# Performance work log

Measured on AMD Instinct MI355X. Metric: run time of the kernel, lower is better.

The kernel has to match this reference:

```python
import jax, jax.numpy as jnp
import numpy as np

B, N, L, H, N_NODE, STEP = 1024, 64, 64, 128, 50000, 2


def setup_inputs() -> dict:
    key = jax.random.key(0)
    ks = jax.random.split(key, 24)
    stdv = 1.0 / np.sqrt(H)
    u = lambda k, shape: jax.random.uniform(k, shape, jnp.float32, -stdv, stdv)
    emb = u(ks[0], (N_NODE + 1, H))
    emb = emb.at[0].set(0.0)  # padding_idx=0
    return {
        "A": jax.random.uniform(ks[1], (B, N, 2 * N), jnp.float32),
        "items": jax.random.randint(ks[2], (B, N), 0, N_NODE + 1, jnp.int32),
        "mask": jnp.ones((B, L), jnp.int32),
        "alias_input": jax.random.randint(ks[3], (B, L), 0, N, jnp.int32),
        "emb": emb,
        "w_in": u(ks[4], (H, H)), "b_in": u(ks[5], (H,)),
        "w_out": u(ks[6], (H, H)), "b_out": u(ks[7], (H,)),
        "b_iah": u(ks[8], (H,)), "b_oah": u(ks[9], (H,)),
        "wi": u(ks[10], (3 * H, 2 * H)), "bi": u(ks[11], (3 * H,)),
        "wh": u(ks[12], (3 * H, H)), "bh": u(ks[13], (3 * H,)),
        "w1": u(ks[14], (H, H)), "b1": u(ks[15], (H,)),
        "w2": u(ks[16], (H, H)), "b2": u(ks[17], (H,)),
        "wq": u(ks[18], (1, H)),
        "w3": u(ks[19], (H, 2 * H)), "b3": u(ks[20], (2 * H,))[:H],
    }


def _gru_cell(A, hidden, p):
    n = A.shape[1]
    h_in = hidden @ p["w_in"].T + p["b_in"]
    h_out = hidden @ p["w_out"].T + p["b_out"]
    input_in = jnp.einsum("bnm,bmh->bnh", A[:, :, :n], h_in) + p["b_iah"]
    input_out = jnp.einsum("bnm,bmh->bnh", A[:, :, n:], h_out) + p["b_oah"]
    input_emb = jnp.concatenate([input_in, input_out], axis=2)  # [B,N,2H]
    gi = input_emb @ p["wi"].T + p["bi"]
    gh = hidden @ p["wh"].T + p["bh"]
    i_r, i_i, i_n = jnp.split(gi, 3, axis=2)
    h_r, h_i, h_n = jnp.split(gh, 3, axis=2)
    update_gate = jax.nn.sigmoid(i_i + h_i)
    reset_gate = jax.nn.sigmoid(i_r + h_r)
    new_gate = jnp.tanh(reset_gate * h_n + i_n)
    return (1.0 - update_gate) * hidden + update_gate * new_gate


def reference(A, items, mask, alias_input, emb, w_in, b_in, w_out, b_out,
              b_iah, b_oah, wi, bi, wh, bh, w1, b1, w2, b2, wq, w3, b3):
    p = dict(w_in=w_in, b_in=b_in, w_out=w_out, b_out=b_out, b_iah=b_iah,
             b_oah=b_oah, wi=wi, bi=bi, wh=wh, bh=bh)
    hidden = emb[items]  # [B,N,H]
    for _ in range(STEP):
        hidden = _gru_cell(A, hidden, p)
    # gather session order: seq_hidden[b, l] = hidden[b, alias_input[b, l]]
    seq_hidden = jnp.take_along_axis(hidden, alias_input[:, :, None], axis=1)  # [B,L,H]
    last = jnp.sum(mask, axis=1) - 1  # [B]
    local_emb = jnp.take_along_axis(seq_hidden, last[:, None, None], axis=1)[:, 0]  # [B,H]
    q1 = (local_emb @ w1.T + b1)[:, None, :]
    q2 = seq_hidden @ w2.T + b2
    alpha = jax.nn.sigmoid(q1 + q2) @ wq.T  # [B,L,1]
    global_emb = jnp.sum(alpha * seq_hidden * mask[:, :, None].astype(seq_hidden.dtype), axis=1)
    return jnp.concatenate([local_emb, global_emb], axis=1) @ w3.T + b3
```

## Files before the change

### kernel.cpp

```cpp
#include <hip/hip_runtime.h>
#include <stdint.h>


#define BDIM 256
#define NB   1024
#define NN   64
#define HH   128
#define SH_STR 136
#define SX_STR 264

#define OFS_WIN  0
#define OFS_WOUT 16384
#define OFS_WI   32768
#define OFS_WH   131072
#define OFS_W2   180224
#define N_FRAGS  24576

typedef short v8s __attribute__((ext_vector_type(8)));
typedef float v4f __attribute__((ext_vector_type(4)));

__device__ __forceinline__ float b2f_lo(uint32_t u){
  union { uint32_t u; float f; } v; v.u = u << 16; return v.f;
}
__device__ __forceinline__ float b2f_hi(uint32_t u){
  union { uint32_t u; float f; } v; v.u = u & 0xffff0000u; return v.f;
}
__device__ __forceinline__ uint16_t f2b(float f){
  union { float f; uint32_t u; } v; v.f = f;
  uint32_t r = v.u + 0x7fffu + ((v.u >> 16) & 1u);
  return (uint16_t)(r >> 16);
}
__device__ __forceinline__ float b2f(uint16_t s){
  union { uint32_t u; float f; } v; v.u = ((uint32_t)s) << 16; return v.f;
}
__device__ __forceinline__ float sig_f(float x){ return 1.0f / (1.0f + __expf(-x)); }
__device__ __forceinline__ float tanh_f(float x){ return 1.0f - 2.0f / (__expf(2.0f*x) + 1.0f); }

__device__ __forceinline__ uint32_t pack2bf(float a, float b){
  union { float f; uint32_t u; } ua, ub; ua.f = a; ub.f = b;
  return __builtin_amdgcn_perm(ub.u + 0x8000u, ua.u + 0x8000u, 0x07060302u);
}

__device__ __forceinline__ v8s pack8(const float* __restrict__ p){
  float4 f0 = *reinterpret_cast<const float4*>(p);
  float4 f1 = *reinterpret_cast<const float4*>(p + 4);
  union { uint32_t u[4]; v8s v; } o;
  o.u[0] = pack2bf(f0.x, f0.y);
  o.u[1] = pack2bf(f0.z, f0.w);
  o.u[2] = pack2bf(f1.x, f1.y);
  o.u[3] = pack2bf(f1.z, f1.w);
  return o.v;
}

__device__ __forceinline__ v8s ldsA(const uint16_t* buf, int stride,
                                    int row_base, int k_base, int r, int q){
  return *reinterpret_cast<const v8s*>(&buf[(row_base + r) * stride + k_base + q * 8]);
}

__device__ __forceinline__ v8s ldfrag(const uint16_t* __restrict__ ws,
                                      int base, int tile, int lane){
  return *reinterpret_cast<const v8s*>(ws + base + (((size_t)tile * 64 + lane) << 3));
}

#define MFMA(a, b, c) __builtin_amdgcn_mfma_f32_16x16x32_bf16((a), (b), (c), 0, 0, 0)

__global__ __launch_bounds__(256) void pack_weights(
    const float* __restrict__ w_in, const float* __restrict__ w_out,
    const float* __restrict__ wi,   const float* __restrict__ wh,
    const float* __restrict__ w2,   uint16_t* __restrict__ ws)
{
  int gid = blockIdx.x * blockDim.x + threadIdx.x;
  if (gid >= N_FRAGS) return;
  const float* W; int C; int fi; int base;
  if (gid < 2048)       { W = w_in;  C = 128; fi = gid;         base = OFS_WIN; }
  else if (gid < 4096)  { W = w_out; C = 128; fi = gid - 2048;  base = OFS_WOUT; }
  else if (gid < 16384) { W = wi;    C = 256; fi = gid - 4096;  base = OFS_WI; }
  else if (gid < 22528) { W = wh;    C = 128; fi = gid - 16384; base = OFS_WH; }
  else                  { W = w2;    C = 128; fi = gid - 22528; base = OFS_W2; }
  int lane = fi & 63;
  int tile = fi >> 6;
  int tc   = C >> 5;
  int tr   = tile / tc, kc = tile - tr * tc;
  int r = lane & 15, q = lane >> 4;
  const float* p = W + (size_t)(tr * 16 + r) * C + kc * 32 + q * 8;
  *reinterpret_cast<v8s*>(ws + base + ((size_t)fi << 3)) = pack8(p);
}

__global__ __launch_bounds__(BDIM, 3) void srgnn_kernel(
    const float* __restrict__ A,
    const int*   __restrict__ items,
    const int*   __restrict__ mask,
    const int*   __restrict__ alias_input,
    const float* __restrict__ emb,
    const float* __restrict__ b_in,  const float* __restrict__ b_out,
    const float* __restrict__ b_iah, const float* __restrict__ b_oah,
    const float* __restrict__ bi,    const float* __restrict__ bh,
    const float* __restrict__ w1,    const float* __restrict__ b1,
    const float* __restrict__ b2,
    const float* __restrict__ wq,
    const float* __restrict__ w3,    const float* __restrict__ b3,
    const uint16_t* __restrict__ ws,
    float* __restrict__ out)
{
  __shared__ __align__(16) uint16_t sH[NN * SH_STR];
  __shared__ __align__(16) uint16_t sX[NN * SX_STR];
  __shared__ int sAliasRow[64], sMaskArr[64];

  float* sF      = reinterpret_cast<float*>(sX);
  float* sQ1v    = sF;
  float* sGlobv  = sF + 128;
  float* sAPartv = sF + 256;
  float* sAlphav = sF + 512;
  float* sP      = sF + 576;

  const int t    = threadIdx.x;
  const int b    = blockIdx.x;
  const int lane = t & 63;
  const int wv   = __builtin_amdgcn_readfirstlane(t >> 6);
  const int r    = lane & 15;
  const int q    = lane >> 4;

  {
    const int* itb = items + b * NN;
    for (int j = t; j < NN * HH; j += BDIM) {
      int n = j >> 7, k = j & 127;
      sH[n * SH_STR + k] = f2b(emb[(size_t)itb[n] * HH + k]);
    }
    if (t < 64) {
      sAliasRow[t] = alias_input[b * 64 + t];
      sMaskArr[t]  = mask[b * 64 + t];
    }
  }

  v8s a2[4][2];
  {
    const int half = wv >> 1;
    #pragma unroll
    for (int mt = 0; mt < 4; ++mt)
      #pragma unroll
      for (int kk = 0; kk < 2; ++kk)
        a2[mt][kk] = pack8(A + (size_t)(b * NN + mt * 16 + r) * (2 * NN)
                             + half * 64 + kk * 32 + q * 8);
  }
  __syncthreads();

  for (int step = 0; step < 2; ++step) {
    {
      v8s a[4][4];
      #pragma unroll
      for (int mt = 0; mt < 4; ++mt)
        #pragma unroll
        for (int kk = 0; kk < 4; ++kk)
          a[mt][kk] = ldsA(sH, SH_STR, mt * 16, kk * 32, r, q);

      const int    wbase = (wv < 2) ? OFS_WIN : OFS_WOUT;
      const float* bsel  = (wv < 2) ? b_in : b_out;
      const int    ntofs = (wv < 2) ? 0 : 8;
      #pragma unroll 2
      for (int i = 0; i < 4; ++i) {
        int nt = wv * 4 + i;
        int tr = nt - ntofs;
        int c  = nt * 16 + r;
        float bini = bsel[tr * 16 + r];
        v4f acc0 = {bini, bini, bini, bini}, acc1 = acc0, acc2 = acc0, acc3 = acc0;
        #pragma unroll
        for (int kk = 0; kk < 4; ++kk) {
          v8s bf = ldfrag(ws, wbase, tr * 4 + kk, lane);
          acc0 = MFMA(a[0][kk], bf, acc0);
          acc1 = MFMA(a[1][kk], bf, acc1);
          acc2 = MFMA(a[2][kk], bf, acc2);
          acc3 = MFMA(a[3][kk], bf, acc3);
        }
        #pragma unroll
        for (int reg = 0; reg < 4; ++reg) {
          sX[(0  + q * 4 + reg) * SX_STR + c] = f2b(acc0[reg]);
          sX[(16 + q * 4 + reg) * SX_STR + c] = f2b(acc1[reg]);
          sX[(32 + q * 4 + reg) * SX_STR + c] = f2b(acc2[reg]);
          sX[(48 + q * 4 + reg) * SX_STR + c] = f2b(acc3[reg]);
        }
      }
    }

    {
      const float* bsel2 = (wv < 2) ? b_iah : b_oah;
      const int    wofs2 = (wv < 2) ? 0 : 128;
      #pragma unroll 1
      for (int i = 0; i < 4; ++i) {
        int nt = wv * 4 + i;
        int c  = nt * 16 + r;
        v8s b0, b1f;
        #pragma unroll
        for (int j = 0; j < 8; ++j) {
          b0[j]  = (short)sX[(q * 8 + j) * SX_STR + c];
          b1f[j] = (short)sX[(32 + q * 8 + j) * SX_STR + c];
        }
        float bini = bsel2[c - wofs2];
        v4f acc0 = {bini, bini, bini, bini}, acc1 = acc0, acc2 = acc0, acc3 = acc0;
        acc0 = MFMA(a2[0][0], b0, acc0); acc0 = MFMA(a2[0][1], b1f, acc0);
        acc1 = MFMA(a2[1][0], b0, acc1); acc1 = MFMA(a2[1][1], b1f, acc1);
        acc2 = MFMA(a2[2][0], b0, acc2); acc2 = MFMA(a2[2][1], b1f, acc2);
        acc3 = MFMA(a2[3][0], b0, acc3); acc3 = MFMA(a2[3][1], b1f, acc3);
        #pragma unroll
        for (int reg = 0; reg < 4; ++reg) {
          sX[(0  + q * 4 + reg) * SX_STR + c] = f2b(acc0[reg]);
          sX[(16 + q * 4 + reg) * SX_STR + c] = f2b(acc1[reg]);
          sX[(32 + q * 4 + reg) * SX_STR + c] = f2b(acc2[reg]);
          sX[(48 + q * 4 + reg) * SX_STR + c] = f2b(acc3[reg]);
        }
      }
    }
    __syncthreads();

    {
      const int h0 = wv * 32;
      uint32_t nhpk[2][8];

      #pragma unroll 1
      for (int u = 0; u < 2; ++u) {
        int h = h0 + u * 16 + r;
        float vR  = bi[h] + bh[h];
        float vI  = bi[128 + h] + bh[128 + h];
        float vNi = bi[256 + h];
        float vNh = bh[256 + h];
        v4f aR[4], aI[4], aNi[4], aNh[4];
        #pragma unroll
        for (int mt = 0; mt < 4; ++mt) {
          aR[mt]  = (v4f){vR, vR, vR, vR};
          aI[mt]  = (v4f){vI, vI, vI, vI};
          aNi[mt] = (v4f){vNi, vNi, vNi, vNi};
          aNh[mt] = (v4f){vNh, vNh, vNh, vNh};
        }
        const int trb = wv * 2 + u;
        #pragma unroll 2
        for (int kk = 0; kk < 8; ++kk) {
          v8s af0 = ldsA(sX, SX_STR, 0,  kk * 32, r, q);
          v8s af1 = ldsA(sX, SX_STR, 16, kk * 32, r, q);
          v8s af2 = ldsA(sX, SX_STR, 32, kk * 32, r, q);
          v8s af3 = ldsA(sX, SX_STR, 48, kk * 32, r, q);
          v8s bR = ldfrag(ws, OFS_WI, (0 * 8 + trb) * 8 + kk, lane);
          v8s bI = ldfrag(ws, OFS_WI, (8 + trb) * 8 + kk, lane);
          v8s bN = ldfrag(ws, OFS_WI, (16 + trb) * 8 + kk, lane);
          aR[0]  = MFMA(af0, bR, aR[0]);  aR[1]  = MFMA(af1, bR, aR[1]);
          aR[2]  = MFMA(af2, bR, aR[2]);  aR[3]  = MFMA(af3, bR, aR[3]);
          aI[0]  = MFMA(af0, bI, aI[0]);  aI[1]  = MFMA(af1, bI, aI[1]);
          aI[2]  = MFMA(af2, bI, aI[2]);  aI[3]  = MFMA(af3, bI, aI[3]);
          aNi[0] = MFMA(af0, bN, aNi[0]); aNi[1] = MFMA(af1, bN, aNi[1]);
          aNi[2] = MFMA(af2, bN, aNi[2]); aNi[3] = MFMA(af3, bN, aNi[3]);
        }
        #pragma unroll 2
        for (int kk = 0; kk < 4; ++kk) {
          v8s af0 = ldsA(sH, SH_STR, 0,  kk * 32, r, q);
          v8s af1 = ldsA(sH, SH_STR, 16, kk * 32, r, q);
          v8s af2 = ldsA(sH, SH_STR, 32, kk * 32, r, q);
          v8s af3 = ldsA(sH, SH_STR, 48, kk * 32, r, q);
          v8s bR = ldfrag(ws, OFS_WH, (0 * 8 + trb) * 4 + kk, lane);
          v8s bI = ldfrag(ws, OFS_WH, (8 + trb) * 4 + kk, lane);
          v8s bN = ldfrag(ws, OFS_WH, (16 + trb) * 4 + kk, lane);
          aR[0]  = MFMA(af0, bR, aR[0]);  aR[1]  = MFMA(af1, bR, aR[1]);
          aR[2]  = MFMA(af2, bR, aR[2]);  aR[3]  = MFMA(af3, bR, aR[3]);
          aI[0]  = MFMA(af0, bI, aI[0]);  aI[1]  = MFMA(af1, bI, aI[1]);
          aI[2]  = MFMA(af2, bI, aI[2]);  aI[3]  = MFMA(af3, bI, aI[3]);
          aNh[0] = MFMA(af0, bN, aNh[0]); aNh[1] = MFMA(af1, bN, aNh[1]);
          aNh[2] = MFMA(af2, bN, aNh[2]); aNh[3] = MFMA(af3, bN, aNh[3]);
        }
        #pragma unroll
        for (int mt = 0; mt < 4; ++mt) {
          #pragma unroll
          for (int rp = 0; rp < 2; ++rp) {
            uint32_t pk = 0;
            #pragma unroll
            for (int e = 0; e < 2; ++e) {
              int reg = rp * 2 + e;
              int row = mt * 16 + q * 4 + reg;
              float z  = sig_f(aI[mt][reg]);
              float rr = sig_f(aR[mt][reg]);
              float gg = tanh_f(fmaf(rr, aNh[mt][reg], aNi[mt][reg]));
              float hp = b2f(sH[row * SH_STR + h]);
              pk |= (uint32_t)f2b(fmaf(z, gg - hp, hp)) << (16 * e);
            }
            nhpk[u][mt * 2 + rp] = pk;
          }
        }
      }
      __syncthreads();

      #pragma unroll
      for (int u = 0; u < 2; ++u) {
        int h = h0 + u * 16 + r;
        #pragma unroll
        for (int mt = 0; mt < 4; ++mt)
          #pragma unroll
          for (int rp = 0; rp < 2; ++rp) {
            uint32_t pk = nhpk[u][mt * 2 + rp];
            int row = mt * 16 + q * 4 + rp * 2;
            sH[row * SH_STR + h]       = (uint16_t)(pk & 0xffff);
            sH[(row + 1) * SH_STR + h] = (uint16_t)(pk >> 16);
          }
      }
    }
    __syncthreads();
  }

  int msum = 0;
  #pragma unroll
  for (int l = 0; l < 64; ++l) msum += sMaskArr[l];
  const int lastRow = sAliasRow[msum - 1];
  const int hh  = t & 127;
  const int seg = t >> 7;

  {
    const float4* w14 = reinterpret_cast<const float4*>(w1 + (size_t)hh * HH + seg * 64);
    const uint2*  lr  = reinterpret_cast<const uint2*>(&sH[lastRow * SH_STR + seg * 64]);
    float a0 = seg ? 0.f : b1[hh], a1 = 0.f, a2v = 0.f, a3 = 0.f;
    #pragma unroll 8
    for (int j = 0; j < 16; ++j) {
      float4 w = w14[j]; uint2 v = lr[j];
      a0  = fmaf(b2f_lo(v.x), w.x, a0);  a1 = fmaf(b2f_hi(v.x), w.y, a1);
      a2v = fmaf(b2f_lo(v.y), w.z, a2v); a3 = fmaf(b2f_hi(v.y), w.w, a3);
    }
    sP[seg * 128 + hh] = (a0 + a1) + (a2v + a3);
  }
  __syncthreads();
  if (t < HH) sQ1v[t] = sP[t] + sP[128 + t];
  __syncthreads();

  {
    v8s a[4][4];
    #pragma unroll
    for (int mt = 0; mt < 4; ++mt) {
      int row = sAliasRow[mt * 16 + r];
      #pragma unroll
      for (int kk = 0; kk < 4; ++kk)
        a[mt][kk] = *reinterpret_cast<const v8s*>(&sH[row * SH_STR + kk * 32 + q * 8]);
    }
    float part[16];
    #pragma unroll
    for (int i = 0; i < 16; ++i) part[i] = 0.f;
    #pragma unroll
    for (int u = 0; u < 2; ++u) {
      int h = wv * 32 + u * 16 + r;
      float binit = sQ1v[h] + b2[h];
      v4f acc[4];
      #pragma unroll
      for (int mt = 0; mt < 4; ++mt) acc[mt] = (v4f){binit, binit, binit, binit};
      #pragma unroll
      for (int kk = 0; kk < 4; ++kk) {
        v8s bf = ldfrag(ws, OFS_W2, (wv * 2 + u) * 4 + kk, lane);
        acc[0] = MFMA(a[0][kk], bf, acc[0]);
        acc[1] = MFMA(a[1][kk], bf, acc[1]);
        acc[2] = MFMA(a[2][kk], bf, acc[2]);
        acc[3] = MFMA(a[3][kk], bf, acc[3]);
      }
      float wqh = wq[h];
      #pragma unroll
      for (int mt = 0; mt < 4; ++mt)
        #pragma unroll
        for (int reg = 0; reg < 4; ++reg)
          part[mt * 4 + reg] += sig_f(acc[mt][reg]) * wqh;
    }
    #pragma unroll
    for (int m = 1; m <= 8; m <<= 1)
      #pragma unroll
      for (int i = 0; i < 16; ++i)
        part[i] += __shfl_xor(part[i], m);
    if (r == 0) {
      #pragma unroll
      for (int mt = 0; mt < 4; ++mt)
        #pragma unroll
        for (int reg = 0; reg < 4; ++reg)
          sAPartv[wv * 64 + mt * 16 + q * 4 + reg] = part[mt * 4 + reg];
    }
  }
  __syncthreads();
  if (t < 64) {
    sAlphav[t] = (sAPartv[t] + sAPartv[64 + t] + sAPartv[128 + t] + sAPartv[192 + t])
               * (float)sMaskArr[t];
  }
  __syncthreads();

  {
    float acc = 0.0f;
    #pragma unroll
    for (int l = 0; l < 32; ++l) {
      int ll = seg * 32 + l;
      acc = fmaf(sAlphav[ll], b2f(sH[sAliasRow[ll] * SH_STR + hh]), acc);
    }
    sP[seg * 128 + hh] = acc;
  }
  __syncthreads();
  if (t < HH) sGlobv[t] = sP[t] + sP[128 + t];
  __syncthreads();

  {
    const float4* w34 = reinterpret_cast<const float4*>(w3 + (size_t)hh * 256 + seg * 128);
    float a0 = seg ? 0.f : b3[hh], a1 = 0.f, a2v = 0.f, a3 = 0.f;
    if (seg == 0) {
      const uint2* lr = reinterpret_cast<const uint2*>(&sH[lastRow * SH_STR]);
      #pragma unroll 8
      for (int j = 0; j < 32; ++j) {
        float4 w = w34[j]; uint2 v = lr[j];
        a0  = fmaf(b2f_lo(v.x), w.x, a0);  a1 = fmaf(b2f_hi(v.x), w.y, a1);
        a2v = fmaf(b2f_lo(v.y), w.z, a2v); a3 = fmaf(b2f_hi(v.y), w.w, a3);
      }
    } else {
      #pragma unroll 8
      for (int j = 0; j < 32; ++j) {
        float4 w = w34[j];
        a0  = fmaf(sGlobv[4*j+0], w.x, a0);  a1 = fmaf(sGlobv[4*j+1], w.y, a1);
        a2v = fmaf(sGlobv[4*j+2], w.z, a2v); a3 = fmaf(sGlobv[4*j+3], w.w, a3);
      }
    }
    sP[seg * 128 + hh] = (a0 + a1) + (a2v + a3);
  }
  __syncthreads();
  if (t < HH) out[b * HH + t] = sP[t] + sP[128 + t];
}

extern "C" void kernel_launch(void* const* d_in, const int* in_sizes, int n_in,
                              void* d_out, int out_size, void* d_ws, size_t ws_size,
                              hipStream_t stream) {
  const float* A          = (const float*)d_in[0];
  const int*   items      = (const int*)  d_in[1];
  const int*   mask       = (const int*)  d_in[2];
  const int*   alias_in   = (const int*)  d_in[3];
  const float* emb        = (const float*)d_in[4];
  const float* w_in       = (const float*)d_in[5];
  const float* b_in       = (const float*)d_in[6];
  const float* w_out      = (const float*)d_in[7];
  const float* b_out      = (const float*)d_in[8];
  const float* b_iah      = (const float*)d_in[9];
  const float* b_oah      = (const float*)d_in[10];
  const float* wi         = (const float*)d_in[11];
  const float* bi         = (const float*)d_in[12];
  const float* wh         = (const float*)d_in[13];
  const float* bh         = (const float*)d_in[14];
  const float* w1         = (const float*)d_in[15];
  const float* b1         = (const float*)d_in[16];
  const float* w2         = (const float*)d_in[17];
  const float* b2         = (const float*)d_in[18];
  const float* wq         = (const float*)d_in[19];
  const float* w3         = (const float*)d_in[20];
  const float* b3         = (const float*)d_in[21];
  float* out = (float*)d_out;
  uint16_t* wsp = (uint16_t*)d_ws;

  hipLaunchKernelGGL(pack_weights, dim3((N_FRAGS + 255) / 256), dim3(256), 0, stream,
                     w_in, w_out, wi, wh, w2, wsp);
  hipLaunchKernelGGL(srgnn_kernel, dim3(NB), dim3(BDIM), 0, stream,
                     A, items, mask, alias_in, emb,
                     b_in, b_out, b_iah, b_oah, bi, bh,
                     w1, b1, b2, wq, w3, b3, wsp, out);
}
```

Baseline: 255.3 us.

## Double block to 512 threads, splitting GRU and tail work across eight waves

Raises the block from four to eight waves and repartitions every stage. Each wave now owns half as many output column tiles in the projection and GRU gate GEMMs, and the w1, alpha and w3 tails are split into four segments with matching shared-memory reductions. The aim is more waves per block to hide MFMA, LDS and global-load latency while each wave uses fewer registers. The cost is that each wave reloads the same A fragments from LDS, adds reduction and barrier overhead, and occupancy now depends on whether six 512-thread blocks actually fit per CU.

After: 385.5 us. +51.0%, slower.

```diff
diff --git a/kernel.cpp b/kernel.cpp
--- a/kernel.cpp
+++ b/kernel.cpp
@@ -2,7 +2,7 @@
 #include <stdint.h>
 
 
-#define BDIM 256
+#define BDIM 512
 #define NB   1024
 #define NN   64
 #define HH   128
@@ -86,7 +86,7 @@
   *reinterpret_cast<v8s*>(ws + base + ((size_t)fi << 3)) = pack8(p);
 }
 
-__global__ __launch_bounds__(BDIM, 3) void srgnn_kernel(
+__global__ __launch_bounds__(BDIM, 6) void srgnn_kernel(
     const float* __restrict__ A,
     const int*   __restrict__ items,
     const int*   __restrict__ mask,
@@ -110,8 +110,8 @@
   float* sQ1v    = sF;
   float* sGlobv  = sF + 128;
   float* sAPartv = sF + 256;
-  float* sAlphav = sF + 512;
-  float* sP      = sF + 576;
+  float* sAlphav = sF + 768;
+  float* sP      = sF + 832;
 
   const int t    = threadIdx.x;
   const int b    = blockIdx.x;
@@ -134,7 +134,7 @@
 
   v8s a2[4][2];
   {
-    const int half = wv >> 1;
+    const int half = wv >> 2;
     #pragma unroll
     for (int mt = 0; mt < 4; ++mt)
       #pragma unroll
@@ -153,12 +153,12 @@
         for (int kk = 0; kk < 4; ++kk)
           a[mt][kk] = ldsA(sH, SH_STR, mt * 16, kk * 32, r, q);
 
-      const int    wbase = (wv < 2) ? OFS_WIN : OFS_WOUT;
-      const float* bsel  = (wv < 2) ? b_in : b_out;
-      const int    ntofs = (wv < 2) ? 0 : 8;
-      #pragma unroll 2
-      for (int i = 0; i < 4; ++i) {
-        int nt = wv * 4 + i;
+      const int    wbase = (wv < 4) ? OFS_WIN : OFS_WOUT;
+      const float* bsel  = (wv < 4) ? b_in : b_out;
+      const int    ntofs = (wv < 4) ? 0 : 8;
+      #pragma unroll
+      for (int i = 0; i < 2; ++i) {
+        int nt = wv * 2 + i;
         int tr = nt - ntofs;
         int c  = nt * 16 + r;
         float bini = bsel[tr * 16 + r];
@@ -182,11 +182,11 @@
     }
 
     {
-      const float* bsel2 = (wv < 2) ? b_iah : b_oah;
-      const int    wofs2 = (wv < 2) ? 0 : 128;
+      const float* bsel2 = (wv < 4) ? b_iah : b_oah;
+      const int    wofs2 = (wv < 4) ? 0 : 128;
       #pragma unroll 1
-      for (int i = 0; i < 4; ++i) {
-        int nt = wv * 4 + i;
+      for (int i = 0; i < 2; ++i) {
+        int nt = wv * 2 + i;
         int c  = nt * 16 + r;
         v8s b0, b1f;
         #pragma unroll
@@ -212,91 +212,83 @@
     __syncthreads();
 
     {
-      const int h0 = wv * 32;
-      uint32_t nhpk[2][8];
-
-      #pragma unroll 1
-      for (int u = 0; u < 2; ++u) {
-        int h = h0 + u * 16 + r;
-        float vR  = bi[h] + bh[h];
-        float vI  = bi[128 + h] + bh[128 + h];
-        float vNi = bi[256 + h];
-        float vNh = bh[256 + h];
-        v4f aR[4], aI[4], aNi[4], aNh[4];
-        #pragma unroll
-        for (int mt = 0; mt < 4; ++mt) {
-          aR[mt]  = (v4f){vR, vR, vR, vR};
-          aI[mt]  = (v4f){vI, vI, vI, vI};
-          aNi[mt] = (v4f){vNi, vNi, vNi, vNi};
-          aNh[mt] = (v4f){vNh, vNh, vNh, vNh};
-        }
-        const int trb = wv * 2 + u;
-        #pragma unroll 2
-        for (int kk = 0; kk < 8; ++kk) {
-          v8s af0 = ldsA(sX, SX_STR, 0,  kk * 32, r, q);
-          v8s af1 = ldsA(sX, SX_STR, 16, kk * 32, r, q);
-          v8s af2 = ldsA(sX, SX_STR, 32, kk * 32, r, q);
-          v8s af3 = ldsA(sX, SX_STR, 48, kk * 32, r, q);
-          v8s bR = ldfrag(ws, OFS_WI, (0 * 8 + trb) * 8 + kk, lane);
-          v8s bI = ldfrag(ws, OFS_WI, (8 + trb) * 8 + kk, lane);
-          v8s bN = ldfrag(ws, OFS_WI, (16 + trb) * 8 + kk, lane);
-          aR[0]  = MFMA(af0, bR, aR[0]);  aR[1]  = MFMA(af1, bR, aR[1]);
-          aR[2]  = MFMA(af2, bR, aR[2]);  aR[3]  = MFMA(af3, bR, aR[3]);
-          aI[0]  = MFMA(af0, bI, aI[0]);  aI[1]  = MFMA(af1, bI, aI[1]);
-          aI[2]  = MFMA(af2, bI, aI[2]);  aI[3]  = MFMA(af3, bI, aI[3]);
-          aNi[0] = MFMA(af0, bN, aNi[0]); aNi[1] = MFMA(af1, bN, aNi[1]);
-          aNi[2] = MFMA(af2, bN, aNi[2]); aNi[3] = MFMA(af3, bN, aNi[3]);
-        }
-        #pragma unroll 2
-        for (int kk = 0; kk < 4; ++kk) {
-          v8s af0 = ldsA(sH, SH_STR, 0,  kk * 32, r, q);
-          v8s af1 = ldsA(sH, SH_STR, 16, kk * 32, r, q);
-          v8s af2 = ldsA(sH, SH_STR, 32, kk * 32, r, q);
-          v8s af3 = ldsA(sH, SH_STR, 48, kk * 32, r, q);
-          v8s bR = ldfrag(ws, OFS_WH, (0 * 8 + trb) * 4 + kk, lane);
-          v8s bI = ldfrag(ws, OFS_WH, (8 + trb) * 4 + kk, lane);
-          v8s bN = ldfrag(ws, OFS_WH, (16 + trb) * 4 + kk, lane);
-          aR[0]  = MFMA(af0, bR, aR[0]);  aR[1]  = MFMA(af1, bR, aR[1]);
-          aR[2]  = MFMA(af2, bR, aR[2]);  aR[3]  = MFMA(af3, bR, aR[3]);
-          aI[0]  = MFMA(af0, bI, aI[0]);  aI[1]  = MFMA(af1, bI, aI[1]);
-          aI[2]  = MFMA(af2, bI, aI[2]);  aI[3]  = MFMA(af3, bI, aI[3]);
-          aNh[0] = MFMA(af0, bN, aNh[0]); aNh[1] = MFMA(af1, bN, aNh[1]);
-          aNh[2] = MFMA(af2, bN, aNh[2]); aNh[3] = MFMA(af3, bN, aNh[3]);
-        }
-        #pragma unroll
-        for (int mt = 0; mt < 4; ++mt) {
+      const int trb = wv;
+      const int h   = wv * 16 + r;
+      uint32_t nhpk[8];
+
+      float vR  = bi[h] + bh[h];
+      float vI  = bi[128 + h] + bh[128 + h];
+      float vNi = bi[256 + h];
+      float vNh = bh[256 + h];
+      v4f aR[4], aI[4], aNi[4], aNh[4];
+      #pragma unroll
+      for (int mt = 0; mt < 4; ++mt) {
+        aR[mt]  = (v4f){vR, vR, vR, vR};
+        aI[mt]  = (v4f){vI, vI, vI, vI};
+        aNi[mt] = (v4f){vNi, vNi, vNi, vNi};
+        aNh[mt] = (v4f){vNh, vNh, vNh, vNh};
+      }
+      #pragma unroll 2
+      for (int kk = 0; kk < 8; ++kk) {
+        v8s af0 = ldsA(sX, SX_STR, 0,  kk * 32, r, q);
+        v8s af1 = ldsA(sX, SX_STR, 16, kk * 32, r, q);
+        v8s af2 = ldsA(sX, SX_STR, 32, kk * 32, r, q);
+        v8s af3 = ldsA(sX, SX_STR, 48, kk * 32, r, q);
+        v8s bR = ldfrag(ws, OFS_WI, (0 * 8 + trb) * 8 + kk, lane);
+        v8s bI = ldfrag(ws, OFS_WI, (8 + trb) * 8 + kk, lane);
+        v8s bN = ldfrag(ws, OFS_WI, (16 + trb) * 8 + kk, lane);
+        aR[0]  = MFMA(af0, bR, aR[0]);  aR[1]  = MFMA(af1, bR, aR[1]);
+        aR[2]  = MFMA(af2, bR, aR[2]);  aR[3]  = MFMA(af3, bR, aR[3]);
+        aI[0]  = MFMA(af0, bI, aI[0]);  aI[1]  = MFMA(af1, bI, aI[1]);
+        aI[2]  = MFMA(af2, bI, aI[2]);  aI[3]  = MFMA(af3, bI, aI[3]);
+        aNi[0] = MFMA(af0, bN, aNi[0]); aNi[1] = MFMA(af1, bN, aNi[1]);
+        aNi[2] = MFMA(af2, bN, aNi[2]); aNi[3] = MFMA(af3, bN, aNi[3]);
+      }
+      #pragma unroll 2
+      for (int kk = 0; kk < 4; ++kk) {
+        v8s af0 = ldsA(sH, SH_STR, 0,  kk * 32, r, q);
+        v8s af1 = ldsA(sH, SH_STR, 16, kk * 32, r, q);
+        v8s af2 = ldsA(sH, SH_STR, 32, kk * 32, r, q);
+        v8s af3 = ldsA(sH, SH_STR, 48, kk * 32, r, q);
+        v8s bR = ldfrag(ws, OFS_WH, (0 * 8 + trb) * 4 + kk, lane);
+        v8s bI = ldfrag(ws, OFS_WH, (8 + trb) * 4 + kk, lane);
+        v8s bN = ldfrag(ws, OFS_WH, (16 + trb) * 4 + kk, lane);
+        aR[0]  = MFMA(af0, bR, aR[0]);  aR[1]  = MFMA(af1, bR, aR[1]);
+        aR[2]  = MFMA(af2, bR, aR[2]);  aR[3]  = MFMA(af3, bR, aR[3]);
+        aI[0]  = MFMA(af0, bI, aI[0]);  aI[1]  = MFMA(af1, bI, aI[1]);
+        aI[2]  = MFMA(af2, bI, aI[2]);  aI[3]  = MFMA(af3, bI, aI[3]);
+        aNh[0] = MFMA(af0, bN, aNh[0]); aNh[1] = MFMA(af1, bN, aNh[1]);
+        aNh[2] = MFMA(af2, bN, aNh[2]); aNh[3] = MFMA(af3, bN, aNh[3]);
+      }
+      #pragma unroll
+      for (int mt = 0; mt < 4; ++mt) {
+        #pragma unroll
+        for (int rp = 0; rp < 2; ++rp) {
+          uint32_t pk = 0;
           #pragma unroll
-          for (int rp = 0; rp < 2; ++rp) {
-            uint32_t pk = 0;
-            #pragma unroll
-            for (int e = 0; e < 2; ++e) {
-              int reg = rp * 2 + e;
-              int row = mt * 16 + q * 4 + reg;
-              float z  = sig_f(aI[mt][reg]);
-              float rr = sig_f(aR[mt][reg]);
-              float gg = tanh_f(fmaf(rr, aNh[mt][reg], aNi[mt][reg]));
-              float hp = b2f(sH[row * SH_STR + h]);
-              pk |= (uint32_t)f2b(fmaf(z, gg - hp, hp)) << (16 * e);
-            }
-            nhpk[u][mt * 2 + rp] = pk;
+          for (int e = 0; e < 2; ++e) {
+            int reg = rp * 2 + e;
+            int row = mt * 16 + q * 4 + reg;
+            float z  = sig_f(aI[mt][reg]);
+            float rr = sig_f(aR[mt][reg]);
+            float gg = tanh_f(fmaf(rr, aNh[mt][reg], aNi[mt][reg]));
+            float hp = b2f(sH[row * SH_STR + h]);
+            pk |= (uint32_t)f2b(fmaf(z, gg - hp, hp)) << (16 * e);
           }
+          nhpk[mt * 2 + rp] = pk;
         }
       }
       __syncthreads();
 
       #pragma unroll
-      for (int u = 0; u < 2; ++u) {
-        int h = h0 + u * 16 + r;
-        #pragma unroll
-        for (int mt = 0; mt < 4; ++mt)
-          #pragma unroll
-          for (int rp = 0; rp < 2; ++rp) {
-            uint32_t pk = nhpk[u][mt * 2 + rp];
-            int row = mt * 16 + q * 4 + rp * 2;
-            sH[row * SH_STR + h]       = (uint16_t)(pk & 0xffff);
-            sH[(row + 1) * SH_STR + h] = (uint16_t)(pk >> 16);
-          }
-      }
+      for (int mt = 0; mt < 4; ++mt)
+        #pragma unroll
+        for (int rp = 0; rp < 2; ++rp) {
+          uint32_t pk = nhpk[mt * 2 + rp];
+          int row = mt * 16 + q * 4 + rp * 2;
+          sH[row * SH_STR + h]       = (uint16_t)(pk & 0xffff);
+          sH[(row + 1) * SH_STR + h] = (uint16_t)(pk >> 16);
+        }
     }
     __syncthreads();
   }
@@ -309,11 +301,11 @@
   const int seg = t >> 7;
 
   {
-    const float4* w14 = reinterpret_cast<const float4*>(w1 + (size_t)hh * HH + seg * 64);
-    const uint2*  lr  = reinterpret_cast<const uint2*>(&sH[lastRow * SH_STR + seg * 64]);
+    const float4* w14 = reinterpret_cast<const float4*>(w1 + (size_t)hh * HH + seg * 32);
+    const uint2*  lr  = reinterpret_cast<const uint2*>(&sH[lastRow * SH_STR + seg * 32]);
     float a0 = seg ? 0.f : b1[hh], a1 = 0.f, a2v = 0.f, a3 = 0.f;
-    #pragma unroll 8
-    for (int j = 0; j < 16; ++j) {
+    #pragma unroll
+    for (int j = 0; j < 8; ++j) {
       float4 w = w14[j]; uint2 v = lr[j];
       a0  = fmaf(b2f_lo(v.x), w.x, a0);  a1 = fmaf(b2f_hi(v.x), w.y, a1);
       a2v = fmaf(b2f_lo(v.y), w.z, a2v); a3 = fmaf(b2f_hi(v.y), w.w, a3);
@@ -321,7 +313,7 @@
     sP[seg * 128 + hh] = (a0 + a1) + (a2v + a3);
   }
   __syncthreads();
-  if (t < HH) sQ1v[t] = sP[t] + sP[128 + t];
+  if (t < HH) sQ1v[t] = (sP[t] + sP[128 + t]) + (sP[256 + t] + sP[384 + t]);
   __syncthreads();
 
   {
@@ -333,31 +325,26 @@
       for (int kk = 0; kk < 4; ++kk)
         a[mt][kk] = *reinterpret_cast<const v8s*>(&sH[row * SH_STR + kk * 32 + q * 8]);
     }
+    const int h = wv * 16 + r;
+    float binit = sQ1v[h] + b2[h];
+    v4f acc[4];
+    #pragma unroll
+    for (int mt = 0; mt < 4; ++mt) acc[mt] = (v4f){binit, binit, binit, binit};
+    #pragma unroll
+    for (int kk = 0; kk < 4; ++kk) {
+      v8s bf = ldfrag(ws, OFS_W2, wv * 4 + kk, lane);
+      acc[0] = MFMA(a[0][kk], bf, acc[0]);
+      acc[1] = MFMA(a[1][kk], bf, acc[1]);
+      acc[2] = MFMA(a[2][kk], bf, acc[2]);
+      acc[3] = MFMA(a[3][kk], bf, acc[3]);
+    }
     float part[16];
-    #pragma unroll
-    for (int i = 0; i < 16; ++i) part[i] = 0.f;
-    #pragma unroll
-    for (int u = 0; u < 2; ++u) {
-      int h = wv * 32 + u * 16 + r;
-      float binit = sQ1v[h] + b2[h];
-      v4f acc[4];
-      #pragma unroll
-      for (int mt = 0; mt < 4; ++mt) acc[mt] = (v4f){binit, binit, binit, binit};
-      #pragma unroll
-      for (int kk = 0; kk < 4; ++kk) {
-        v8s bf = ldfrag(ws, OFS_W2, (wv * 2 + u) * 4 + kk, lane);
-        acc[0] = MFMA(a[0][kk], bf, acc[0]);
-        acc[1] = MFMA(a[1][kk], bf, acc[1]);
-        acc[2] = MFMA(a[2][kk], bf, acc[2]);
-        acc[3] = MFMA(a[3][kk], bf, acc[3]);
-      }
-      float wqh = wq[h];
-      #pragma unroll
-      for (int mt = 0; mt < 4; ++mt)
-        #pragma unroll
-        for (int reg = 0; reg < 4; ++reg)
-          part[mt * 4 + reg] += sig_f(acc[mt][reg]) * wqh;
-    }
+    float wqh = wq[h];
+    #pragma unroll
+    for (int mt = 0; mt < 4; ++mt)
+      #pragma unroll
+      for (int reg = 0; reg < 4; ++reg)
+        part[mt * 4 + reg] = sig_f(acc[mt][reg]) * wqh;
     #pragma unroll
     for (int m = 1; m <= 8; m <<= 1)
       #pragma unroll
@@ -373,47 +360,51 @@
   }
   __syncthreads();
   if (t < 64) {
-    sAlphav[t] = (sAPartv[t] + sAPartv[64 + t] + sAPartv[128 + t] + sAPartv[192 + t])
-               * (float)sMaskArr[t];
+    float a = 0.f;
+    #pragma unroll
+    for (int w8 = 0; w8 < 8; ++w8) a += sAPartv[w8 * 64 + t];
+    sAlphav[t] = a * (float)sMaskArr[t];
   }
   __syncthreads();
 
   {
     float acc = 0.0f;
     #pragma unroll
-    for (int l = 0; l < 32; ++l) {
-      int ll = seg * 32 + l;
+    for (int l = 0; l < 16; ++l) {
+      int ll = seg * 16 + l;
       acc = fmaf(sAlphav[ll], b2f(sH[sAliasRow[ll] * SH_STR + hh]), acc);
     }
     sP[seg * 128 + hh] = acc;
   }
   __syncthreads();
-  if (t < HH) sGlobv[t] = sP[t] + sP[128 + t];
-  __syncthreads();
-
-  {
-    const float4* w34 = reinterpret_cast<const float4*>(w3 + (size_t)hh * 256 + seg * 128);
+  if (t < HH) sGlobv[t] = (sP[t] + sP[128 + t]) + (sP[256 + t] + sP[384 + t]);
+  __syncthreads();
+
+  {
+    const float4* w34 = reinterpret_cast<const float4*>(w3 + (size_t)hh * 256 + seg * 64);
     float a0 = seg ? 0.f : b3[hh], a1 = 0.f, a2v = 0.f, a3 = 0.f;
-    if (seg == 0) {
-      const uint2* lr = reinterpret_cast<const uint2*>(&sH[lastRow * SH_STR]);
-      #pragma unroll 8
-      for (int j = 0; j < 32; ++j) {
+    if (seg < 2) {
+      const uint2* lr = reinterpret_cast<const uint2*>(&sH[lastRow * SH_STR + seg * 64]);
+      #pragma unroll
+      for (int j = 0; j < 16; ++j) {
         float4 w = w34[j]; uint2 v = lr[j];
         a0  = fmaf(b2f_lo(v.x), w.x, a0);  a1 = fmaf(b2f_hi(v.x), w.y, a1);
         a2v = fmaf(b2f_lo(v.y), w.z, a2v); a3 = fmaf(b2f_hi(v.y), w.w, a3);
       }
     } else {
-      #pragma unroll 8
-      for (int j = 0; j < 32; ++j) {
+      const float* gp = sGlobv + (seg - 2) * 64;
+      #pragma unroll
+      for (int j = 0; j < 16; ++j) {
         float4 w = w34[j];
-        a0  = fmaf(sGlobv[4*j+0], w.x, a0);  a1 = fmaf(sGlobv[4*j+1], w.y, a1);
-        a2v = fmaf(sGlobv[4*j+2], w.z, a2v); a3 = fmaf(sGlobv[4*j+3], w.w, a3);
+        a0  = fmaf(gp[4*j+0], w.x, a0);  a1 = fmaf(gp[4*j+1], w.y, a1);
+        a2v = fmaf(gp[4*j+2], w.z, a2v); a3 = fmaf(gp[4*j+3], w.w, a3);
       }
     }
     sP[seg * 128 + hh] = (a0 + a1) + (a2v + a3);
   }
   __syncthreads();
-  if (t < HH) out[b * HH + t] = sP[t] + sP[128 + t];
+  if (t < HH)
+    out[b * HH + t] = (sP[t] + sP[128 + t]) + (sP[256 + t] + sP[384 + t]);
 }
 
 extern "C" void kernel_launch(void* const* d_in, const int* in_sizes, int n_in,
```
